# Kernel optimization log

Measured on AMD Instinct MI355X. Metric: run time of the kernel, lower is better.

The kernel has to match this reference:

```python
import jax, jax.numpy as jnp
import numpy as np

B, P, H, N, D, K = 1024, 1024, 4096, 32, 512, 128


def setup_inputs() -> dict:
    key = jax.random.key(0)
    k1, k2, k3, k4, k5 = jax.random.split(key, 5)
    return {
        "proximal_input": jax.random.normal(k1, (B, P), dtype=jnp.float32),
        "distal_input": jax.random.normal(k2, (B, D), dtype=jnp.float32),
        "W": jax.random.normal(k3, (H, P), dtype=jnp.float32) / np.sqrt(P),
        "b": jax.random.normal(k4, (H,), dtype=jnp.float32) / np.sqrt(P),
        "distal": jax.random.normal(k5, (H, N, D), dtype=jnp.float32),
        "k": K,
    }


def reference(proximal_input, distal_input, W, b, distal, k):
    # proximal path: standard linear -> (B, H)
    proximal_output = proximal_input @ W.T + b
    # per-hidden-unit dendrite projections -> (H, B, N)
    distal_output = jnp.einsum('bd,hnd->hbn', distal_input, distal)
    # pick dominant dendrite by absolute value, keep its signed value
    abs_max_idx = jnp.argmax(jnp.abs(distal_output), axis=-1)          # (H, B)
    distal_max = jnp.take_along_axis(
        distal_output, abs_max_idx[..., None], axis=-1)[..., 0].T      # (B, H)
    # sigmoid gate modulates proximal activations
    result = proximal_output * jax.nn.sigmoid(distal_max)              # (B, H)
    # keep only top-k per row (scatter-built 0/1 mask, as in the original)
    _, top_idxs = jax.lax.top_k(result, k)                             # (B, k)
    rows = jnp.arange(result.shape[0])[:, None]
    mask = jnp.zeros_like(result).at[rows, top_idxs].set(1.0)
    return result * mask
```

## Files before the change

kernel.cpp:

```cpp
#include <hip/hip_runtime.h>
#include <cstdint>
#include <cmath>

#define Bsz  1024
#define Pdim 1024
#define Hdim 4096
#define Ndim 32
#define Ddim 512
#define Ktop 128

typedef _Float16 f16x8  __attribute__((ext_vector_type(8)));
typedef float    f32x16 __attribute__((ext_vector_type(16)));

#define GLDS(gsrc, ldst)                                                        \
  __builtin_amdgcn_global_load_lds(                                             \
      (const __attribute__((address_space(1))) unsigned int*)(gsrc),            \
      (__attribute__((address_space(3))) unsigned int*)(ldst), 16, 0, 0)

#define WS_NEEDED 270532608ull

__global__ __launch_bounds__(256) void convert_img(
    const float* __restrict__ src, char* __restrict__ dst, int kcbits)
{
  const int gid  = blockIdx.x * 256 + threadIdx.x;
  const int row  = gid >> kcbits;
  const int e    = (gid & ((1 << kcbits) - 1)) * 8;
  const int Krow = 8 << kcbits;
  float4 v0 = *(const float4*)(src + (size_t)row * Krow + e);
  float4 v1 = *(const float4*)(src + (size_t)row * Krow + e + 4);
  const int tile = row >> 7, r = row & 127, ks = e >> 5, k = e & 31;
  char* base = dst + (size_t)(tile * (Krow >> 5) + ks) * 16384;
  const int off = ((r >> 5) * 2 + (k >> 4)) * 1024
                + ((r & 31) + 32 * ((k >> 3) & 1)) * 16;
  const float f[8] = {v0.x, v0.y, v0.z, v0.w, v1.x, v1.y, v1.z, v1.w};
  f16x8 hi, lo;
#pragma unroll
  for (int j = 0; j < 8; j++) {
    const _Float16 h = (_Float16)f[j];
    hi[j] = h;
    lo[j] = (_Float16)((f[j] - (float)h) * 256.f);
  }
  *(f16x8*)(base + off)        = hi;
  *(f16x8*)(base + 8192 + off) = lo;
}

#define PIPE_LOOP(NH)                                                           \
  STAGE(0);                                                                     \
  STAGE(1);                                                                     \
  for (int h = 0; h < (NH); ++h) {                                              \
    if (h + 2 < (NH)) {                                                         \
      STAGE(h + 2);                                                             \
      asm volatile("s_waitcnt vmcnt(8)" ::: "memory");                          \
    } else if (h + 1 < (NH)) {                                                  \
      asm volatile("s_waitcnt vmcnt(4)" ::: "memory");                          \
    } else {                                                                    \
      asm volatile("s_waitcnt vmcnt(0)" ::: "memory");                          \
    }                                                                           \
    __builtin_amdgcn_s_barrier();                                               \
    asm volatile("" ::: "memory");                                              \
    const char* buf = lds[h & 3];                                               \
    f16x8 ah[2], al[2], bh[2], bl[2];                                           \
    _Pragma("unroll")                                                           \
    for (int mi = 0; mi < 2; mi++) {                                            \
      const int m = wr * 2 + mi;                                                \
      ah[mi] = *(const f16x8*)(buf + m * 1024 + lane * 16);                     \
      al[mi] = *(const f16x8*)(buf + 4096 + m * 1024 + lane * 16);              \
    }                                                                           \
    _Pragma("unroll")                                                           \
    for (int ni = 0; ni < 2; ni++) {                                            \
      const int m = wc * 2 + ni;                                                \
      bh[ni] = *(const f16x8*)(buf + 8192 + m * 1024 + lane * 16);              \
      bl[ni] = *(const f16x8*)(buf + 12288 + m * 1024 + lane * 16);             \
    }                                                                           \
    __builtin_amdgcn_s_setprio(1);                                              \
    _Pragma("unroll")                                                           \
    for (int ni = 0; ni < 2; ni++)                                              \
      _Pragma("unroll")                                                         \
      for (int mi = 0; mi < 2; mi++) {                                          \
        acc[mi][ni]  = __builtin_amdgcn_mfma_f32_32x32x16_f16(ah[mi], bh[ni], acc[mi][ni],  0, 0, 0); \
        accx[mi][ni] = __builtin_amdgcn_mfma_f32_32x32x16_f16(ah[mi], bl[ni], accx[mi][ni], 0, 0, 0); \
        accx[mi][ni] = __builtin_amdgcn_mfma_f32_32x32x16_f16(al[mi], bh[ni], accx[mi][ni], 0, 0, 0); \
      }                                                                         \
    __builtin_amdgcn_s_setprio(0);                                              \
  }

__global__ __launch_bounds__(256, 2) void proximal_mfma(
    const char* __restrict__ Aw, const char* __restrict__ Bw,
    const float* __restrict__ bias, float* __restrict__ out)
{
  __shared__ __align__(16) char lds[4][16384];
  const int t = threadIdx.x, lane = t & 63, wv = t >> 6;
  const int hi32 = lane >> 5, c31 = lane & 31;
  const int wr = wv >> 1, wc = wv & 1;

  const int blk = blockIdx.x;
  const int xcd = blk & 7, q = blk >> 3;
  const int htile = xcd * 4 + (q >> 3);
  const int btile = q & 7;
  const int h0 = htile * 128, b0 = btile * 128;

  f32x16 acc[2][2], accx[2][2];
#pragma unroll
  for (int mi = 0; mi < 2; mi++)
#pragma unroll
    for (int ni = 0; ni < 2; ni++) {
      acc[mi][ni]  = (f32x16)(0.f);
      accx[mi][ni] = (f32x16)(0.f);
    }

  const char* Abase = Aw + (size_t)(htile * 32) * 16384;
  const char* Bbase = Bw + (size_t)(btile * 32) * 16384;

  auto STAGE = [&](int h) {
    const int ks = h >> 1, kk = h & 1;
    char* buf = lds[h & 3];
    const char* Ai = Abase + (size_t)ks * 16384;
    const char* Bi = Bbase + (size_t)ks * 16384;
    const char* srcs[4] = {Ai, Ai + 8192, Bi, Bi + 8192};
#pragma unroll
    for (int j = 0; j < 4; j++) {
      const int c = j * 4 + wv;
      GLDS(srcs[j] + (wv * 2 + kk) * 1024 + lane * 16,
           buf + c * 1024 + lane * 16);
    }
  };

  PIPE_LOOP(64)

#pragma unroll
  for (int mi = 0; mi < 2; ++mi)
#pragma unroll
    for (int ni = 0; ni < 2; ++ni) {
      const int bcol = b0 + wc * 64 + ni * 32 + c31;
#pragma unroll
      for (int qq = 0; qq < 4; ++qq) {
        const int hb = h0 + wr * 64 + mi * 32 + qq * 8 + hi32 * 4;
        const float4 bb = *(const float4*)(bias + hb);
        float4 o;
        o.x = acc[mi][ni][4*qq+0] + accx[mi][ni][4*qq+0] * 0.00390625f + bb.x;
        o.y = acc[mi][ni][4*qq+1] + accx[mi][ni][4*qq+1] * 0.00390625f + bb.y;
        o.z = acc[mi][ni][4*qq+2] + accx[mi][ni][4*qq+2] * 0.00390625f + bb.z;
        o.w = acc[mi][ni][4*qq+3] + accx[mi][ni][4*qq+3] * 0.00390625f + bb.w;
        *(float4*)(out + (size_t)bcol * Hdim + hb) = o;
      }
    }
}

__global__ __launch_bounds__(256, 2) void distal_mfma(
    const char* __restrict__ Aw, const char* __restrict__ Bw,
    float* __restrict__ out)
{
  __shared__ __align__(16) char lds[4][16384];
  const int t = threadIdx.x, lane = t & 63, wv = t >> 6;
  const int hi32 = lane >> 5, c31 = lane & 31;
  const int wr = wv >> 1, wc = wv & 1;

  const int blk = blockIdx.x;
  const int xcd = blk & 7, q = blk >> 3;
  const int ntile = xcd * 128 + (q >> 3);
  const int btile = q & 7;

  f32x16 acc[2][2], accx[2][2];
#pragma unroll
  for (int mi = 0; mi < 2; mi++)
#pragma unroll
    for (int ni = 0; ni < 2; ni++) {
      acc[mi][ni]  = (f32x16)(0.f);
      accx[mi][ni] = (f32x16)(0.f);
    }

  const char* Abase = Aw + (size_t)(ntile * 16) * 16384;
  const char* Bbase = Bw + (size_t)(btile * 16) * 16384;

  auto STAGE = [&](int h) {
    const int ks = h >> 1, kk = h & 1;
    char* buf = lds[h & 3];
    const char* Ai = Abase + (size_t)ks * 16384;
    const char* Bi = Bbase + (size_t)ks * 16384;
    const char* srcs[4] = {Ai, Ai + 8192, Bi, Bi + 8192};
#pragma unroll
    for (int j = 0; j < 4; j++) {
      const int c = j * 4 + wv;
      GLDS(srcs[j] + (wv * 2 + kk) * 1024 + lane * 16,
           buf + c * 1024 + lane * 16);
    }
  };

  PIPE_LOOP(32)

#pragma unroll
  for (int mi = 0; mi < 2; ++mi)
#pragma unroll
    for (int ni = 0; ni < 2; ++ni) {
      float bestA = -1.f, bestV = 0.f;
      int   bestN = 999;
#pragma unroll
      for (int reg = 0; reg < 16; ++reg) {
        const float v = acc[mi][ni][reg] + accx[mi][ni][reg] * 0.00390625f;
        const float a = fabsf(v);
        const int   n = (reg & 3) + 8 * (reg >> 2) + 4 * hi32;
        if (a > bestA) { bestA = a; bestV = v; bestN = n; }
      }
      {
        const float oa = __shfl_xor(bestA, 32, 64);
        const float ov = __shfl_xor(bestV, 32, 64);
        const int   on = __shfl_xor(bestN, 32, 64);
        if (oa > bestA || (oa == bestA && on < bestN)) {
          bestA = oa; bestV = ov; bestN = on;
        }
      }
      if (hi32 == 0) {
        const int bcol = btile * 128 + wc * 64 + ni * 32 + c31;
        const int h    = ntile * 4 + wr * 2 + mi;
        const float gate = 1.f / (1.f + expf(-bestV));
        out[(size_t)bcol * Hdim + h] *= gate;
      }
    }
}

__global__ __launch_bounds__(256) void proximal_gemm(
    const float* __restrict__ pin, const float* __restrict__ W,
    const float* __restrict__ bias, float* __restrict__ out)
{
  __shared__ float Blds[32 * 256];
  __shared__ float Alds[32 * 32];
  const int t  = threadIdx.x;
  const int l  = t & 63;
  const int wv = t >> 6;
  const int ell   = blockIdx.x;
  const int xcd   = ell & 7;
  const int q     = ell >> 3;
  const int htile = xcd * 2 + (q >> 5);
  const int btile = q & 31;
  const int h0 = htile * 256, b0 = btile * 32;

  float acc[8][4];
#pragma unroll
  for (int i = 0; i < 8; i++)
    for (int j = 0; j < 4; j++) acc[i][j] = 0.f;

  const float* wrow = W + (size_t)(h0 + t) * Pdim;
  const int ab = t >> 3, ak = (t & 7) * 4;
  const float* arow = pin + (size_t)(b0 + ab) * Pdim + ak;

  for (int kt = 0; kt < Pdim / 32; ++kt) {
    const int p0 = kt * 32;
    float wbuf[32];
#pragma unroll
    for (int f = 0; f < 8; f++) {
      float4 v = *(const float4*)(wrow + p0 + f * 4);
      wbuf[f * 4 + 0] = v.x; wbuf[f * 4 + 1] = v.y;
      wbuf[f * 4 + 2] = v.z; wbuf[f * 4 + 3] = v.w;
    }
    float4 av = *(const float4*)(arow + p0);
    __syncthreads();
#pragma unroll
    for (int f = 0; f < 32; f++) Blds[f * 256 + t] = wbuf[f];
    Alds[(ak + 0) * 32 + ab] = av.x;
    Alds[(ak + 1) * 32 + ab] = av.y;
    Alds[(ak + 2) * 32 + ab] = av.z;
    Alds[(ak + 3) * 32 + ab] = av.w;
    __syncthreads();
#pragma unroll
    for (int k = 0; k < 32; k++) {
      float4 bv  = *(const float4*)&Blds[k * 256 + 4 * l];
      float4 alo = *(const float4*)&Alds[k * 32 + 8 * wv];
      float4 ahi = *(const float4*)&Alds[k * 32 + 8 * wv + 4];
      float a0[8] = {alo.x, alo.y, alo.z, alo.w, ahi.x, ahi.y, ahi.z, ahi.w};
#pragma unroll
      for (int i = 0; i < 8; i++) {
        acc[i][0] += a0[i] * bv.x;
        acc[i][1] += a0[i] * bv.y;
        acc[i][2] += a0[i] * bv.z;
        acc[i][3] += a0[i] * bv.w;
      }
    }
  }
  float4 bb = *(const float4*)(bias + h0 + 4 * l);
#pragma unroll
  for (int i = 0; i < 8; i++) {
    float4 o;
    o.x = acc[i][0] + bb.x;
    o.y = acc[i][1] + bb.y;
    o.z = acc[i][2] + bb.z;
    o.w = acc[i][3] + bb.w;
    *(float4*)(out + (size_t)(b0 + 8 * wv + i) * Hdim + h0 + 4 * l) = o;
  }
}

__global__ __launch_bounds__(256) void distal_gate_fb(
    const float* __restrict__ din, const float* __restrict__ distal,
    float* __restrict__ out)
{
  __shared__ float Blds[32 * 256];
  __shared__ float Alds[32 * 32];
  const int t  = threadIdx.x;
  const int l  = t & 63;
  const int wv = t >> 6;
  const int ell   = blockIdx.x;
  const int xcd   = ell & 7;
  const int q     = ell >> 3;
  const int htile = xcd * 64 + (q >> 5);
  const int btile = q & 31;
  const int n0 = htile * 256, b0 = btile * 32;

  float acc[8][4];
#pragma unroll
  for (int i = 0; i < 8; i++)
    for (int j = 0; j < 4; j++) acc[i][j] = 0.f;

  const float* brow = distal + (size_t)(n0 + t) * Ddim;
  const int ab = t >> 3, ak = (t & 7) * 4;
  const float* arow = din + (size_t)(b0 + ab) * Ddim + ak;

  for (int kt = 0; kt < Ddim / 32; ++kt) {
    const int d0 = kt * 32;
    float wbuf[32];
#pragma unroll
    for (int f = 0; f < 8; f++) {
      float4 v = *(const float4*)(brow + d0 + f * 4);
      wbuf[f * 4 + 0] = v.x; wbuf[f * 4 + 1] = v.y;
      wbuf[f * 4 + 2] = v.z; wbuf[f * 4 + 3] = v.w;
    }
    float4 av = *(const float4*)(arow + d0);
    __syncthreads();
#pragma unroll
    for (int f = 0; f < 32; f++) Blds[f * 256 + t] = wbuf[f];
    Alds[(ak + 0) * 32 + ab] = av.x;
    Alds[(ak + 1) * 32 + ab] = av.y;
    Alds[(ak + 2) * 32 + ab] = av.z;
    Alds[(ak + 3) * 32 + ab] = av.w;
    __syncthreads();
#pragma unroll
    for (int k = 0; k < 32; k++) {
      float4 bv  = *(const float4*)&Blds[k * 256 + 4 * l];
      float4 alo = *(const float4*)&Alds[k * 32 + 8 * wv];
      float4 ahi = *(const float4*)&Alds[k * 32 + 8 * wv + 4];
      float a0[8] = {alo.x, alo.y, alo.z, alo.w, ahi.x, ahi.y, ahi.z, ahi.w};
#pragma unroll
      for (int i = 0; i < 8; i++) {
        acc[i][0] += a0[i] * bv.x;
        acc[i][1] += a0[i] * bv.y;
        acc[i][2] += a0[i] * bv.z;
        acc[i][3] += a0[i] * bv.w;
      }
    }
  }
  const int i0  = l & 7;
  const int grp = l >> 3;
  float v = 0.f;
#pragma unroll
  for (int bi = 0; bi < 8; bi++) {
    float bav = fabsf(acc[bi][0]);
    float bv_ = acc[bi][0];
    int   bn  = 4 * i0;
#pragma unroll
    for (int j = 1; j < 4; j++) {
      float av2 = fabsf(acc[bi][j]);
      if (av2 > bav) { bav = av2; bv_ = acc[bi][j]; bn = 4 * i0 + j; }
    }
#pragma unroll
    for (int m = 1; m < 8; m <<= 1) {
      float oav = __shfl_xor(bav, m, 64);
      float ov  = __shfl_xor(bv_, m, 64);
      int   on  = __shfl_xor(bn,  m, 64);
      if (oav > bav || (oav == bav && on < bn)) { bav = oav; bv_ = ov; bn = on; }
    }
    if (bi == i0) v = bv_;
  }
  const float gate = 1.f / (1.f + expf(-v));
  const size_t idx = (size_t)(b0 + 8 * wv + i0) * Hdim + (size_t)htile * 8 + grp;
  out[idx] *= gate;
}

__device__ __forceinline__ unsigned keyf(float f) {
  unsigned u = __float_as_uint(f);
  return (u & 0x80000000u) ? ~u : (u | 0x80000000u);
}

__global__ __launch_bounds__(256) void topk_mask(float* __restrict__ out)
{
  __shared__ float vals[Hdim];
  __shared__ unsigned hist[256];
  __shared__ unsigned sc[4];
  __shared__ unsigned s_prefix, s_kk;
  const int t = threadIdx.x;
  float* row = out + (size_t)blockIdx.x * Hdim;

#pragma unroll
  for (int qq = 0; qq < 4; qq++) {
    float4 v = *(const float4*)(row + qq * 1024 + t * 4);
    *(float4*)&vals[qq * 1024 + t * 4] = v;
  }
  if (t == 0) { s_prefix = 0u; s_kk = Ktop; }
  __syncthreads();

  for (int shift = 24; shift >= 0; shift -= 8) {
    hist[t] = 0u;
    __syncthreads();
    const unsigned prefix = s_prefix;
    const unsigned maskhi = (shift == 24) ? 0u : (0xFFFFFFFFu << (shift + 8));
    for (int c = 0; c < 16; c++) {
      unsigned u = keyf(vals[c * 256 + t]);
      if ((u & maskhi) == prefix)
        atomicAdd(&hist[(u >> shift) & 255u], 1u);
    }
    __syncthreads();
    if (t == 0) {
      unsigned kk = s_kk, cum = 0;
      int bin = 255;
      for (; bin > 0; --bin) {
        unsigned c = hist[bin];
        if (cum + c >= kk) break;
        cum += c;
      }
      s_kk = kk - cum;
      s_prefix = prefix | ((unsigned)bin << shift);
    }
    __syncthreads();
  }
  const unsigned T  = s_prefix;
  const unsigned kk = s_kk;

  const int lane = t & 63, w = t >> 6;
  unsigned running = 0;
  for (int c = 0; c < 16; c++) {
    const int h = c * 256 + t;
    const float v = vals[h];
    const unsigned u = keyf(v);
    const bool tie = (u == T);
    unsigned long long m = __ballot(tie);
    unsigned lpfx = (unsigned)__popcll(m & ((1ull << lane) - 1ull));
    if (lane == 0) sc[w] = (unsigned)__popcll(m);
    __syncthreads();
    unsigned off = 0;
#pragma unroll
    for (int ww = 0; ww < 4; ww++) if (ww < w) off += sc[ww];
    const unsigned rank = running + off + lpfx;
    row[h] = (u > T) ? v : ((tie && rank < kk) ? v : 0.f);
    const unsigned tot = sc[0] + sc[1] + sc[2] + sc[3];
    __syncthreads();
    running += tot;
  }
}

extern "C" void kernel_launch(void* const* d_in, const int* in_sizes, int n_in,
                              void* d_out, int out_size, void* d_ws, size_t ws_size,
                              hipStream_t stream)
{
  (void)in_sizes; (void)n_in; (void)out_size;
  const float* pin  = (const float*)d_in[0];
  const float* dinp = (const float*)d_in[1];
  const float* W    = (const float*)d_in[2];
  const float* bias = (const float*)d_in[3];
  const float* dst  = (const float*)d_in[4];
  float* out = (float*)d_out;

  if (ws_size >= WS_NEEDED) {
    char* ws = (char*)d_ws;
    hipLaunchKernelGGL(convert_img,   dim3(2048),  dim3(256), 0, stream, W,   ws,             7);
    hipLaunchKernelGGL(convert_img,   dim3(512),   dim3(256), 0, stream, pin, ws + 16777216,  7);
    hipLaunchKernelGGL(proximal_mfma, dim3(256),   dim3(256), 0, stream, ws, ws + 16777216, bias, out);
    hipLaunchKernelGGL(convert_img,   dim3(32768), dim3(256), 0, stream, dst,  ws,             6);
    hipLaunchKernelGGL(convert_img,   dim3(256),   dim3(256), 0, stream, dinp, ws + 268435456, 6);
    hipLaunchKernelGGL(distal_mfma,   dim3(8192),  dim3(256), 0, stream, ws, ws + 268435456, out);
  } else {
    hipLaunchKernelGGL(proximal_gemm, dim3(512),   dim3(256), 0, stream, pin, W, bias, out);
    hipLaunchKernelGGL(distal_gate_fb, dim3(16384), dim3(256), 0, stream, dinp, dst, out);
  }

  hipLaunchKernelGGL(topk_mask, dim3(Bsz), dim3(256), 0, stream, out);
}
```

Before: 615.1 us.

## Use per-wave private LDS for A and direct register loads for B, removing barriers

Rewrites the GEMM pipeline so each wave stages its own A fragments into a private LDS region and loads B fragments straight from global memory into registers, double-buffered across iterations. This removes the block-wide s_barrier and shared LDS tiles, aiming to cut synchronisation stalls and let waves run independently. The cost is that data once shared through LDS is now loaded redundantly by several waves, which raises global/L2 traffic. B loads also become plain vector loads whose latency must be hidden by the vmcnt-based schedule.

```diff
diff --git a/kernel.cpp b/kernel.cpp
--- a/kernel.cpp
+++ b/kernel.cpp
@@ -44,54 +44,66 @@
   *(f16x8*)(base + 8192 + off) = lo;
 }
 
-#define PIPE_LOOP(NH)                                                           \
-  STAGE(0);                                                                     \
-  STAGE(1);                                                                     \
-  for (int h = 0; h < (NH); ++h) {                                              \
-    if (h + 2 < (NH)) {                                                         \
-      STAGE(h + 2);                                                             \
-      asm volatile("s_waitcnt vmcnt(8)" ::: "memory");                          \
-    } else if (h + 1 < (NH)) {                                                  \
-      asm volatile("s_waitcnt vmcnt(4)" ::: "memory");                          \
-    } else {                                                                    \
-      asm volatile("s_waitcnt vmcnt(0)" ::: "memory");                          \
-    }                                                                           \
-    __builtin_amdgcn_s_barrier();                                               \
-    asm volatile("" ::: "memory");                                              \
-    const char* buf = lds[h & 3];                                               \
-    f16x8 ah[2], al[2], bh[2], bl[2];                                           \
-    _Pragma("unroll")                                                           \
-    for (int mi = 0; mi < 2; mi++) {                                            \
-      const int m = wr * 2 + mi;                                                \
-      ah[mi] = *(const f16x8*)(buf + m * 1024 + lane * 16);                     \
-      al[mi] = *(const f16x8*)(buf + 4096 + m * 1024 + lane * 16);              \
-    }                                                                           \
-    _Pragma("unroll")                                                           \
-    for (int ni = 0; ni < 2; ni++) {                                            \
-      const int m = wc * 2 + ni;                                                \
-      bh[ni] = *(const f16x8*)(buf + 8192 + m * 1024 + lane * 16);              \
-      bl[ni] = *(const f16x8*)(buf + 12288 + m * 1024 + lane * 16);             \
-    }                                                                           \
+#define VMWAIT(N)                                            \
+  asm volatile("s_waitcnt vmcnt(" #N ")" ::: "memory");      \
+  __builtin_amdgcn_sched_barrier(0)
+
+#define LOADB(H, BH, BL)                                                        \
+  { const char* sB = Bwave + (size_t)((H) >> 1) * 16384 + ((H) & 1) * 1024 + lane16; \
+    BH[0] = *(const f16x8*)(sB);                                                \
+    BH[1] = *(const f16x8*)(sB + 2048);                                         \
+    BL[0] = *(const f16x8*)(sB + 8192);                                         \
+    BL[1] = *(const f16x8*)(sB + 8192 + 2048);                                  \
+    __builtin_amdgcn_sched_barrier(0); }
+
+#define STAGE_A(H)                                                              \
+  { char* dA = priv + ((H) & 3) * 4096;                                         \
+    const char* sA = Awave + (size_t)((H) >> 1) * 16384 + ((H) & 1) * 1024 + lane16; \
+    GLDS(sA,                dA);                                                \
+    GLDS(sA + 2048,         dA + 1024);                                         \
+    GLDS(sA + 8192,         dA + 2048);                                         \
+    GLDS(sA + 8192 + 2048,  dA + 3072); }
+
+#define COMPUTE(H, BH, BL)                                                      \
+  { const char* buf = priv + ((H) & 3) * 4096 + lane16;                         \
+    f16x8 ah[2], al[2];                                                         \
+    ah[0] = *(const f16x8*)(buf);                                               \
+    ah[1] = *(const f16x8*)(buf + 1024);                                        \
+    al[0] = *(const f16x8*)(buf + 2048);                                        \
+    al[1] = *(const f16x8*)(buf + 3072);                                        \
     __builtin_amdgcn_s_setprio(1);                                              \
     _Pragma("unroll")                                                           \
     for (int ni = 0; ni < 2; ni++)                                              \
       _Pragma("unroll")                                                         \
       for (int mi = 0; mi < 2; mi++) {                                          \
-        acc[mi][ni]  = __builtin_amdgcn_mfma_f32_32x32x16_f16(ah[mi], bh[ni], acc[mi][ni],  0, 0, 0); \
-        accx[mi][ni] = __builtin_amdgcn_mfma_f32_32x32x16_f16(ah[mi], bl[ni], accx[mi][ni], 0, 0, 0); \
-        accx[mi][ni] = __builtin_amdgcn_mfma_f32_32x32x16_f16(al[mi], bh[ni], accx[mi][ni], 0, 0, 0); \
+        acc[mi][ni]  = __builtin_amdgcn_mfma_f32_32x32x16_f16(ah[mi], BH[ni], acc[mi][ni],  0, 0, 0); \
+        accx[mi][ni] = __builtin_amdgcn_mfma_f32_32x32x16_f16(ah[mi], BL[ni], accx[mi][ni], 0, 0, 0); \
+        accx[mi][ni] = __builtin_amdgcn_mfma_f32_32x32x16_f16(al[mi], BH[ni], accx[mi][ni], 0, 0, 0); \
       }                                                                         \
-    __builtin_amdgcn_s_setprio(0);                                              \
-  }
+    __builtin_amdgcn_s_setprio(0); }
+
+#define PIPE_LOOP(NH)                                                           \
+  f16x8 bh0[2], bl0[2], bh1[2], bl1[2];                                         \
+  LOADB(0, bh0, bl0);                                                           \
+  STAGE_A(0); STAGE_A(1);                                                       \
+  int h = 0;                                                                    \
+  for (; h + 3 < (NH); h += 2) {                                                \
+    LOADB(h + 1, bh1, bl1); STAGE_A(h + 2); VMWAIT(12); COMPUTE(h, bh0, bl0);   \
+    LOADB(h + 2, bh0, bl0); STAGE_A(h + 3); VMWAIT(12); COMPUTE(h + 1, bh1, bl1); \
+  }                                                                             \
+  LOADB(h + 1, bh1, bl1); VMWAIT(8); COMPUTE(h, bh0, bl0);                      \
+  VMWAIT(0); COMPUTE(h + 1, bh1, bl1);
 
 __global__ __launch_bounds__(256, 2) void proximal_mfma(
     const char* __restrict__ Aw, const char* __restrict__ Bw,
     const float* __restrict__ bias, float* __restrict__ out)
 {
-  __shared__ __align__(16) char lds[4][16384];
+  __shared__ __align__(16) char lds[4][4][4096];
   const int t = threadIdx.x, lane = t & 63, wv = t >> 6;
+  const int lane16 = lane * 16;
   const int hi32 = lane >> 5, c31 = lane & 31;
   const int wr = wv >> 1, wc = wv & 1;
+  char* priv = &lds[wv][0][0];
 
   const int blk = blockIdx.x;
   const int xcd = blk & 7, q = blk >> 3;
@@ -108,22 +120,8 @@
       accx[mi][ni] = (f32x16)(0.f);
     }
 
-  const char* Abase = Aw + (size_t)(htile * 32) * 16384;
-  const char* Bbase = Bw + (size_t)(btile * 32) * 16384;
-
-  auto STAGE = [&](int h) {
-    const int ks = h >> 1, kk = h & 1;
-    char* buf = lds[h & 3];
-    const char* Ai = Abase + (size_t)ks * 16384;
-    const char* Bi = Bbase + (size_t)ks * 16384;
-    const char* srcs[4] = {Ai, Ai + 8192, Bi, Bi + 8192};
-#pragma unroll
-    for (int j = 0; j < 4; j++) {
-      const int c = j * 4 + wv;
-      GLDS(srcs[j] + (wv * 2 + kk) * 1024 + lane * 16,
-           buf + c * 1024 + lane * 16);
-    }
-  };
+  const char* Awave = Aw + (size_t)(htile * 32) * 16384 + wr * 4096;
+  const char* Bwave = Bw + (size_t)(btile * 32) * 16384 + wc * 4096;
 
   PIPE_LOOP(64)
 
@@ -150,10 +148,12 @@
     const char* __restrict__ Aw, const char* __restrict__ Bw,
     float* __restrict__ out)
 {
-  __shared__ __align__(16) char lds[4][16384];
+  __shared__ __align__(16) char lds[4][4][4096];
   const int t = threadIdx.x, lane = t & 63, wv = t >> 6;
+  const int lane16 = lane * 16;
   const int hi32 = lane >> 5, c31 = lane & 31;
   const int wr = wv >> 1, wc = wv & 1;
+  char* priv = &lds[wv][0][0];
 
   const int blk = blockIdx.x;
   const int xcd = blk & 7, q = blk >> 3;
@@ -169,22 +169,8 @@
       accx[mi][ni] = (f32x16)(0.f);
     }
 
-  const char* Abase = Aw + (size_t)(ntile * 16) * 16384;
-  const char* Bbase = Bw + (size_t)(btile * 16) * 16384;
-
-  auto STAGE = [&](int h) {
-    const int ks = h >> 1, kk = h & 1;
-    char* buf = lds[h & 3];
-    const char* Ai = Abase + (size_t)ks * 16384;
-    const char* Bi = Bbase + (size_t)ks * 16384;
-    const char* srcs[4] = {Ai, Ai + 8192, Bi, Bi + 8192};
-#pragma unroll
-    for (int j = 0; j < 4; j++) {
-      const int c = j * 4 + wv;
-      GLDS(srcs[j] + (wv * 2 + kk) * 1024 + lane * 16,
-           buf + c * 1024 + lane * 16);
-    }
-  };
+  const char* Awave = Aw + (size_t)(ntile * 16) * 16384 + wr * 4096;
+  const char* Bwave = Bw + (size_t)(btile * 16) * 16384 + wc * 4096;
 
   PIPE_LOOP(32)
 
```

After: 696.0 us. +13.1%, slower.
